# Kernel tuning notes

Hardware: AMD Instinct MI355X
Metric: run time of the kernel (lower is better)

## Reference

```python
import jax, jax.numpy as jnp
import numpy as np

N = 2_097_152  # total atoms
G = 32_768     # number of graphs (~64 atoms each)
EPS = 1e-4     # sign-detection threshold from the original code


def setup_inputs() -> dict:
    key = jax.random.key(0)
    k1, k2 = jax.random.split(key)
    pos = jax.random.normal(k1, (N, 3), dtype=jnp.float32) * 3.0
    batch = jnp.sort(jax.random.randint(k2, (N,), 0, G))
    return {"pos": pos, "batch": batch, "num_graphs": G}


def reference(pos, batch, num_graphs):
    n = pos.shape[0]
    dtype = pos.dtype

    # per-graph centroid (scatter_mean)
    counts = jax.ops.segment_sum(jnp.ones((n,), dtype), batch, num_segments=num_graphs)
    center = jax.ops.segment_sum(pos, batch, num_segments=num_graphs) / jnp.maximum(counts, 1.0)[:, None]
    pc = pos - center[batch]                      # [N,3] centered positions

    # per-atom inertia contribution: r^2 * I - p p^T, then scatter_add per graph
    r_sq = jnp.sum(pc * pc, axis=-1)              # [N]
    outer = jnp.einsum('ni,nj->nij', pc, pc)      # [N,3,3]
    I_atom = r_sq[:, None, None] * jnp.eye(3, dtype=dtype) - outer
    I_mol = jax.ops.segment_sum(I_atom, batch, num_segments=num_graphs)  # [G,3,3]

    L, Q = jnp.linalg.eigh(I_mol)                 # Q: [G,3,3], columns = principal axes

    # projections of centered positions onto the (pre-flip) eigenbasis.
    # NOTE: in the torch loop, p_proj is computed once before any sign flips, and
    # flipping column 0 does not affect p_proj[:,1], so axes 0 and 1 are independent.
    proj = jnp.einsum('ni,nij->nj', pc, Q[batch])  # [N,3]

    idx = jnp.arange(n)

    def axis_sign(a):
        # parallel "first atom (in original order) with |proj| > EPS" per graph
        qual = jnp.abs(proj[:, a]) > EPS
        key_idx = jnp.where(qual, idx, n)
        first = jax.ops.segment_min(key_idx, batch, num_segments=num_graphs)  # [G]
        found = first < n
        val = proj[jnp.minimum(first, n - 1), a]
        return jnp.where(found & (val < 0), -1.0, 1.0).astype(dtype)

    s0 = axis_sign(0)
    s1 = axis_sign(1)
    q0 = Q[:, :, 0] * s0[:, None]
    q1 = Q[:, :, 1] * s1[:, None]
    q2 = jnp.cross(q0, q1)  # enforce right-handed frame
    return jnp.stack([q0, q1, q2], axis=-1)       # [G,3,3]
```

## Files before the change

### kernel.cpp

```cpp
#include <hip/hip_runtime.h>
#include <math.h>

#define CANON_EPS 1e-4f

__global__ __launch_bounds__(256) void moments_kernel(
    const float* __restrict__ pos, const int* __restrict__ batch,
    int* __restrict__ wsi, float* __restrict__ wsf, int n, int G) {
  int tid = (int)(blockIdx.x * (unsigned)blockDim.x + threadIdx.x);
  int gid = tid >> 3;
  int sub = tid & 7;
  int lane = (int)(threadIdx.x & 63u);
  if (gid >= G) return;

  int target = gid + (sub & 1);
  int lo = 0, hi = n;
  while (lo < hi) {
    int mid = (lo + hi) >> 1;
    bool less = batch[mid] < target;
    lo = less ? mid + 1 : lo;
    hi = less ? hi : mid;
  }
  int base = lane & ~7;
  int s = __shfl(lo, base);
  int e = __shfl(lo, base + 1);
  if (sub == 0) wsi[gid] = s;
  if (sub == 1 && gid == G - 1) wsi[G] = lo;

  int cnt = e - s;

  float sx = 0.f, sy = 0.f, sz = 0.f;
  float sxx = 0.f, syy = 0.f, szz = 0.f, sxy = 0.f, sxz = 0.f, syz = 0.f;
  for (int i = s + sub; i < e; i += 8) {
    float x = pos[3 * i + 0];
    float y = pos[3 * i + 1];
    float z = pos[3 * i + 2];
    sx += x; sy += y; sz += z;
    sxx = fmaf(x, x, sxx); syy = fmaf(y, y, syy); szz = fmaf(z, z, szz);
    sxy = fmaf(x, y, sxy); sxz = fmaf(x, z, sxz); syz = fmaf(y, z, syz);
  }
#define RED8(v)                                                              \
  v += __shfl_xor(v, 1); v += __shfl_xor(v, 2); v += __shfl_xor(v, 4);
  RED8(sx) RED8(sy) RED8(sz)
  RED8(sxx) RED8(syy) RED8(szz)
  RED8(sxy) RED8(sxz) RED8(syz)
#undef RED8

  float fn = (float)(cnt > 0 ? cnt : 1);
  float inv = 1.0f / fn;
  float mx = sx * inv, my = sy * inv, mz = sz * inv;
  float Sxx = fmaf(-fn * mx, mx, sxx);
  float Syy = fmaf(-fn * my, my, syy);
  float Szz = fmaf(-fn * mz, mz, szz);
  float Sxy = fmaf(-fn * mx, my, sxy);
  float Sxz = fmaf(-fn * mx, mz, sxz);
  float Syz = fmaf(-fn * my, mz, syz);

  float v = mx;
  v = (sub == 1) ? my : v;
  v = (sub == 2) ? mz : v;
  v = (sub == 3) ? (Syy + Szz) : v;
  v = (sub == 4) ? (Sxx + Szz) : v;
  v = (sub == 5) ? (Sxx + Syy) : v;
  v = (sub == 6) ? (-Sxy) : v;
  v = (sub == 7) ? (-Sxz) : v;
  wsf[sub * G + gid] = v;
  if (sub == 0) wsf[8 * G + gid] = -Syz;
}

__device__ __forceinline__ void jacobi3_f32(float a00, float a11, float a22,
                                            float a01, float a02, float a12,
                                            float Q[3][3]) {
  float A00 = a00, A11 = a11, A22 = a22;
  float A01 = a01, A02 = a02, A12 = a12;
  float Q00 = 1.f, Q01 = 0.f, Q02 = 0.f;
  float Q10 = 0.f, Q11 = 1.f, Q12 = 0.f;
  float Q20 = 0.f, Q21 = 0.f, Q22 = 1.f;

#define ROT(App, Aqq, Apq, Akp, Akq, Qrp0, Qrq0, Qrp1, Qrq1, Qrp2, Qrq2)     \
  {                                                                          \
    float apq = Apq;                                                         \
    float theta = (Aqq - App) / (2.0f * apq);                                \
    float t = copysignf(1.0f, theta) /                                       \
              (fabsf(theta) + sqrtf(1.0f + theta * theta));                  \
    t = (apq == 0.0f) ? 0.0f : t;                    \
    float c = 1.0f / sqrtf(1.0f + t * t);                                    \
    float s = t * c;                                                         \
    App = App - t * apq;                                                     \
    Aqq = Aqq + t * apq;                                                     \
    Apq = 0.0f;                                                              \
    float akp = Akp, akq = Akq;                                              \
    Akp = c * akp - s * akq;                                                 \
    Akq = s * akp + c * akq;                                                 \
    float r0p = Qrp0, r0q = Qrq0;                                            \
    Qrp0 = c * r0p - s * r0q;                                                \
    Qrq0 = s * r0p + c * r0q;                                                \
    float r1p = Qrp1, r1q = Qrq1;                                            \
    Qrp1 = c * r1p - s * r1q;                                                \
    Qrq1 = s * r1p + c * r1q;                                                \
    float r2p = Qrp2, r2q = Qrq2;                                            \
    Qrp2 = c * r2p - s * r2q;                                                \
    Qrq2 = s * r2p + c * r2q;                                                \
  }

#pragma unroll
  for (int sweep = 0; sweep < 5; ++sweep) {
    ROT(A00, A11, A01, A02, A12, Q00, Q01, Q10, Q11, Q20, Q21);
    ROT(A00, A22, A02, A01, A12, Q00, Q02, Q10, Q12, Q20, Q22);
    ROT(A11, A22, A12, A01, A02, Q01, Q02, Q11, Q12, Q21, Q22);
  }
#undef ROT

  float w0 = A00, w1 = A11, w2 = A22;
#define CSWAP(wa, wb, qa0, qb0, qa1, qb1, qa2, qb2)                          \
  {                                                                          \
    bool sw = (wb) < (wa);                                                   \
    float tw = wa; wa = sw ? wb : wa; wb = sw ? tw : wb;                     \
    float t0 = qa0; qa0 = sw ? qb0 : qa0; qb0 = sw ? t0 : qb0;               \
    float t1 = qa1; qa1 = sw ? qb1 : qa1; qb1 = sw ? t1 : qb1;               \
    float t2 = qa2; qa2 = sw ? qb2 : qa2; qb2 = sw ? t2 : qb2;               \
  }
  CSWAP(w0, w1, Q00, Q01, Q10, Q11, Q20, Q21);
  CSWAP(w1, w2, Q01, Q02, Q11, Q12, Q21, Q22);
  CSWAP(w0, w1, Q00, Q01, Q10, Q11, Q20, Q21);
#undef CSWAP

  Q[0][0] = Q00; Q[0][1] = Q01; Q[0][2] = Q02;
  Q[1][0] = Q10; Q[1][1] = Q11; Q[1][2] = Q12;
  Q[2][0] = Q20; Q[2][1] = Q21; Q[2][2] = Q22;
}

__global__ __launch_bounds__(256) void eigen_kernel(
    const float* __restrict__ pos, const int* __restrict__ wsi,
    const float* __restrict__ wsf, float* __restrict__ out, int G) {
  int g = (int)(blockIdx.x * (unsigned)blockDim.x + threadIdx.x);
  if (g >= G) return;

  int s = wsi[g];
  int e = wsi[g + 1];

  float cx  = wsf[0 * G + g];
  float cy  = wsf[1 * G + g];
  float cz  = wsf[2 * G + g];
  float ixx = wsf[3 * G + g];
  float iyy = wsf[4 * G + g];
  float izz = wsf[5 * G + g];
  float ixy = wsf[6 * G + g];
  float ixz = wsf[7 * G + g];
  float iyz = wsf[8 * G + g];

  float Q[3][3];
  jacobi3_f32(ixx, iyy, izz, ixy, ixz, iyz, Q);

  float q00 = Q[0][0], q10 = Q[1][0], q20 = Q[2][0];
  float q01 = Q[0][1], q11 = Q[1][1], q21 = Q[2][1];

  bool found0 = false, found1 = false;
  float v0 = 0.f, v1 = 0.f;
  for (int i = s; i < e; ++i) {
    float x = pos[3 * i + 0] - cx;
    float y = pos[3 * i + 1] - cy;
    float z = pos[3 * i + 2] - cz;
    float p0 = x * q00 + y * q10 + z * q20;
    float p1 = x * q01 + y * q11 + z * q21;
    if (!found0 && fabsf(p0) > CANON_EPS) { v0 = p0; found0 = true; }
    if (!found1 && fabsf(p1) > CANON_EPS) { v1 = p1; found1 = true; }
    if (found0 && found1) break;
  }
  float s0 = (found0 && v0 < 0.f) ? -1.f : 1.f;
  float s1 = (found1 && v1 < 0.f) ? -1.f : 1.f;

  float q0x = q00 * s0, q0y = q10 * s0, q0z = q20 * s0;
  float q1x = q01 * s1, q1y = q11 * s1, q1z = q21 * s1;
  float q2x = q0y * q1z - q0z * q1y;
  float q2y = q0z * q1x - q0x * q1z;
  float q2z = q0x * q1y - q0y * q1x;
  float* o = out + (size_t)g * 9;
  o[0] = q0x; o[1] = q1x; o[2] = q2x;
  o[3] = q0y; o[4] = q1y; o[5] = q2y;
  o[6] = q0z; o[7] = q1z; o[8] = q2z;
}

extern "C" void kernel_launch(void* const* d_in, const int* in_sizes, int n_in,
                              void* d_out, int out_size, void* d_ws, size_t ws_size,
                              hipStream_t stream) {
  const float* pos = (const float*)d_in[0];
  const int* batch = (const int*)d_in[1];
  float* out = (float*)d_out;

  int n = in_sizes[0] / 3;
  int G = out_size / 9;

  int* wsi = (int*)d_ws;
  float* wsf = (float*)((char*)d_ws + (((size_t)(G + 1) * 4 + 255) & ~255ull));

  int blocksA = (G * 8 + 255) / 256;
  moments_kernel<<<blocksA, 256, 0, stream>>>(pos, batch, wsi, wsf, n, G);

  eigen_kernel<<<(G + 255) / 256, 256, 0, stream>>>(pos, wsi, wsf, out, G);
}
```

Baseline: 23.46 us.

## Replace per-graph binary search moments with atom-parallel segmented atomic accumulation

Moments are now computed by scanning atoms in fixed chunks of 16 per thread with vectorized loads. Each thread keeps running sums per segment and flushes them to per-graph accumulators with atomics, and it writes segment boundaries where the graph id changes. This removes the per-graph binary searches and the strided, poorly coalesced loads. The centroid and inertia finalization moves into the eigen kernel, which now launches with 64-thread blocks. In exchange it adds a zeroing kernel launch, atomic contention on graphs that span chunk boundaries, and float summation order that varies between runs.

After: 70.15 us. 2.99x slower.

```diff
diff --git a/kernel.cpp b/kernel.cpp
--- a/kernel.cpp
+++ b/kernel.cpp
@@ -2,69 +2,90 @@
 #include <math.h>
 
 #define CANON_EPS 1e-4f
+#define KPT 16
+
+__global__ __launch_bounds__(256) void zero_ws_kernel(float* __restrict__ wsf,
+                                                      int total) {
+  int i = (int)(blockIdx.x * (unsigned)blockDim.x + threadIdx.x);
+  if (i < total) wsf[i] = 0.0f;
+}
 
 __global__ __launch_bounds__(256) void moments_kernel(
     const float* __restrict__ pos, const int* __restrict__ batch,
     int* __restrict__ wsi, float* __restrict__ wsf, int n, int G) {
-  int tid = (int)(blockIdx.x * (unsigned)blockDim.x + threadIdx.x);
-  int gid = tid >> 3;
-  int sub = tid & 7;
-  int lane = (int)(threadIdx.x & 63u);
-  if (gid >= G) return;
-
-  int target = gid + (sub & 1);
-  int lo = 0, hi = n;
-  while (lo < hi) {
-    int mid = (lo + hi) >> 1;
-    bool less = batch[mid] < target;
-    lo = less ? mid + 1 : lo;
-    hi = less ? hi : mid;
-  }
-  int base = lane & ~7;
-  int s = __shfl(lo, base);
-  int e = __shfl(lo, base + 1);
-  if (sub == 0) wsi[gid] = s;
-  if (sub == 1 && gid == G - 1) wsi[G] = lo;
-
-  int cnt = e - s;
+  int t = (int)(blockIdx.x * (unsigned)blockDim.x + threadIdx.x);
+  int i0 = t * KPT;
+  if (i0 >= n) return;
+
+  int pb = (i0 > 0) ? batch[i0 - 1] : -1;
 
   float sx = 0.f, sy = 0.f, sz = 0.f;
   float sxx = 0.f, syy = 0.f, szz = 0.f, sxy = 0.f, sxz = 0.f, syz = 0.f;
-  for (int i = s + sub; i < e; i += 8) {
-    float x = pos[3 * i + 0];
-    float y = pos[3 * i + 1];
-    float z = pos[3 * i + 2];
-    sx += x; sy += y; sz += z;
-    sxx = fmaf(x, x, sxx); syy = fmaf(y, y, syy); szz = fmaf(z, z, szz);
-    sxy = fmaf(x, y, sxy); sxz = fmaf(x, z, sxz); syz = fmaf(y, z, syz);
-  }
-#define RED8(v)                                                              \
-  v += __shfl_xor(v, 1); v += __shfl_xor(v, 2); v += __shfl_xor(v, 4);
-  RED8(sx) RED8(sy) RED8(sz)
-  RED8(sxx) RED8(syy) RED8(szz)
-  RED8(sxy) RED8(sxz) RED8(syz)
-#undef RED8
-
-  float fn = (float)(cnt > 0 ? cnt : 1);
-  float inv = 1.0f / fn;
-  float mx = sx * inv, my = sy * inv, mz = sz * inv;
-  float Sxx = fmaf(-fn * mx, mx, sxx);
-  float Syy = fmaf(-fn * my, my, syy);
-  float Szz = fmaf(-fn * mz, mz, szz);
-  float Sxy = fmaf(-fn * mx, my, sxy);
-  float Sxz = fmaf(-fn * mx, mz, sxz);
-  float Syz = fmaf(-fn * my, mz, syz);
-
-  float v = mx;
-  v = (sub == 1) ? my : v;
-  v = (sub == 2) ? mz : v;
-  v = (sub == 3) ? (Syy + Szz) : v;
-  v = (sub == 4) ? (Sxx + Szz) : v;
-  v = (sub == 5) ? (Sxx + Syy) : v;
-  v = (sub == 6) ? (-Sxy) : v;
-  v = (sub == 7) ? (-Sxz) : v;
-  wsf[sub * G + gid] = v;
-  if (sub == 0) wsf[8 * G + gid] = -Syz;
+  int cur = pb;
+
+#define FLUSH()                                                              \
+  if (cur >= 0) {                                                            \
+    atomicAdd(&wsf[0 * G + cur], sx);                                        \
+    atomicAdd(&wsf[1 * G + cur], sy);                                        \
+    atomicAdd(&wsf[2 * G + cur], sz);                                        \
+    atomicAdd(&wsf[3 * G + cur], sxx);                                       \
+    atomicAdd(&wsf[4 * G + cur], syy);                                       \
+    atomicAdd(&wsf[5 * G + cur], szz);                                       \
+    atomicAdd(&wsf[6 * G + cur], sxy);                                       \
+    atomicAdd(&wsf[7 * G + cur], sxz);                                       \
+    atomicAdd(&wsf[8 * G + cur], syz);                                       \
+  }
+
+  if (i0 + KPT <= n) {
+    int B[KPT];
+#pragma unroll
+    for (int q = 0; q < KPT / 4; ++q) {
+      int4 b4 = *reinterpret_cast<const int4*>(batch + i0 + 4 * q);
+      B[4 * q + 0] = b4.x; B[4 * q + 1] = b4.y;
+      B[4 * q + 2] = b4.z; B[4 * q + 3] = b4.w;
+    }
+    float P[3 * KPT];
+#pragma unroll
+    for (int q = 0; q < 3 * KPT / 4; ++q) {
+      float4 p4 = *reinterpret_cast<const float4*>(pos + (size_t)3 * i0 + 4 * q);
+      P[4 * q + 0] = p4.x; P[4 * q + 1] = p4.y;
+      P[4 * q + 2] = p4.z; P[4 * q + 3] = p4.w;
+    }
+#pragma unroll
+    for (int k = 0; k < KPT; ++k) {
+      int bk = B[k];
+      if (bk != cur) {
+        for (int g = cur + 1; g <= bk; ++g) wsi[g] = i0 + k;
+        FLUSH();
+        sx = sy = sz = sxx = syy = szz = sxy = sxz = syz = 0.f;
+        cur = bk;
+      }
+      float x = P[3 * k + 0], y = P[3 * k + 1], z = P[3 * k + 2];
+      sx += x; sy += y; sz += z;
+      sxx = fmaf(x, x, sxx); syy = fmaf(y, y, syy); szz = fmaf(z, z, szz);
+      sxy = fmaf(x, y, sxy); sxz = fmaf(x, z, sxz); syz = fmaf(y, z, syz);
+    }
+  } else {
+    for (int i = i0; i < n; ++i) {
+      int bk = batch[i];
+      if (bk != cur) {
+        for (int g = cur + 1; g <= bk; ++g) wsi[g] = i;
+        FLUSH();
+        sx = sy = sz = sxx = syy = szz = sxy = sxz = syz = 0.f;
+        cur = bk;
+      }
+      float x = pos[3 * i + 0], y = pos[3 * i + 1], z = pos[3 * i + 2];
+      sx += x; sy += y; sz += z;
+      sxx = fmaf(x, x, sxx); syy = fmaf(y, y, syy); szz = fmaf(z, z, szz);
+      sxy = fmaf(x, y, sxy); sxz = fmaf(x, z, sxz); syz = fmaf(y, z, syz);
+    }
+  }
+  FLUSH();
+#undef FLUSH
+
+  if (i0 + KPT >= n) {
+    for (int g = cur + 1; g <= G; ++g) wsi[g] = n;
+  }
 }
 
 __device__ __forceinline__ void jacobi3_f32(float a00, float a11, float a22,
@@ -129,7 +150,7 @@
   Q[2][0] = Q20; Q[2][1] = Q21; Q[2][2] = Q22;
 }
 
-__global__ __launch_bounds__(256) void eigen_kernel(
+__global__ __launch_bounds__(64) void eigen_kernel(
     const float* __restrict__ pos, const int* __restrict__ wsi,
     const float* __restrict__ wsf, float* __restrict__ out, int G) {
   int g = (int)(blockIdx.x * (unsigned)blockDim.x + threadIdx.x);
@@ -137,16 +158,34 @@
 
   int s = wsi[g];
   int e = wsi[g + 1];
-
-  float cx  = wsf[0 * G + g];
-  float cy  = wsf[1 * G + g];
-  float cz  = wsf[2 * G + g];
-  float ixx = wsf[3 * G + g];
-  float iyy = wsf[4 * G + g];
-  float izz = wsf[5 * G + g];
-  float ixy = wsf[6 * G + g];
-  float ixz = wsf[7 * G + g];
-  float iyz = wsf[8 * G + g];
+  int cnt = e - s;
+
+  float sx  = wsf[0 * G + g];
+  float sy  = wsf[1 * G + g];
+  float sz  = wsf[2 * G + g];
+  float sxx = wsf[3 * G + g];
+  float syy = wsf[4 * G + g];
+  float szz = wsf[5 * G + g];
+  float sxy = wsf[6 * G + g];
+  float sxz = wsf[7 * G + g];
+  float syz = wsf[8 * G + g];
+
+  float fn = (float)(cnt > 0 ? cnt : 1);
+  float inv = 1.0f / fn;
+  float mx = sx * inv, my = sy * inv, mz = sz * inv;
+  float Sxx = fmaf(-fn * mx, mx, sxx);
+  float Syy = fmaf(-fn * my, my, syy);
+  float Szz = fmaf(-fn * mz, mz, szz);
+  float Sxy = fmaf(-fn * mx, my, sxy);
+  float Sxz = fmaf(-fn * mx, mz, sxz);
+  float Syz = fmaf(-fn * my, mz, syz);
+
+  float ixx = Syy + Szz;
+  float iyy = Sxx + Szz;
+  float izz = Sxx + Syy;
+  float ixy = -Sxy;
+  float ixz = -Sxz;
+  float iyz = -Syz;
 
   float Q[3][3];
   jacobi3_f32(ixx, iyy, izz, ixy, ixz, iyz, Q);
@@ -157,9 +196,9 @@
   bool found0 = false, found1 = false;
   float v0 = 0.f, v1 = 0.f;
   for (int i = s; i < e; ++i) {
-    float x = pos[3 * i + 0] - cx;
-    float y = pos[3 * i + 1] - cy;
-    float z = pos[3 * i + 2] - cz;
+    float x = pos[3 * i + 0] - mx;
+    float y = pos[3 * i + 1] - my;
+    float z = pos[3 * i + 2] - mz;
     float p0 = x * q00 + y * q10 + z * q20;
     float p1 = x * q01 + y * q11 + z * q21;
     if (!found0 && fabsf(p0) > CANON_EPS) { v0 = p0; found0 = true; }
@@ -193,8 +232,12 @@
   int* wsi = (int*)d_ws;
   float* wsf = (float*)((char*)d_ws + (((size_t)(G + 1) * 4 + 255) & ~255ull));
 
-  int blocksA = (G * 8 + 255) / 256;
-  moments_kernel<<<blocksA, 256, 0, stream>>>(pos, batch, wsi, wsf, n, G);
-
-  eigen_kernel<<<(G + 255) / 256, 256, 0, stream>>>(pos, wsi, wsf, out, G);
-}
+  int totalf = 9 * G;
+  zero_ws_kernel<<<(totalf + 255) / 256, 256, 0, stream>>>(wsf, totalf);
+
+  int threadsA = (n + KPT - 1) / KPT;
+  moments_kernel<<<(threadsA + 255) / 256, 256, 0, stream>>>(pos, batch, wsi,
+                                                             wsf, n, G);
+
+  eigen_kernel<<<(G + 63) / 64, 64, 0, stream>>>(pos, wsi, wsf, out, G);
+}
```

## Precompute segment starts in a scan kernel and widen per-graph moment reduction

Applied to the files above, without the earlier changes.

Replaces the per-graph binary search over batch with a separate kernel that writes segment start offsets by comparing adjacent batch entries. The moments kernel now uses 16 lanes per graph with a predicated, unrolled first pass, and the eigen kernel's sign search loads atoms four at a time. This removes dependent search latency but adds a full pass over batch and an extra kernel launch.

Result: faster. 22.73 us (-3.1%).

```diff
diff --git a/kernel.cpp b/kernel.cpp
--- a/kernel.cpp
+++ b/kernel.cpp
@@ -3,34 +3,47 @@
 
 #define CANON_EPS 1e-4f
 
+__global__ __launch_bounds__(256) void build_starts_kernel(
+    const int* __restrict__ batch, int* __restrict__ wsi, int n, int G) {
+  int i = (int)(blockIdx.x * (unsigned)blockDim.x + threadIdx.x);
+  if (i >= n) return;
+  int b = batch[i];
+  int bp = (i == 0) ? -1 : batch[i - 1];
+  for (int g = bp + 1; g <= b; ++g) wsi[g] = i;
+  if (i == n - 1) {
+    for (int g = b + 1; g <= G; ++g) wsi[G > g ? g : G] = n;
+  }
+}
+
 __global__ __launch_bounds__(256) void moments_kernel(
-    const float* __restrict__ pos, const int* __restrict__ batch,
-    int* __restrict__ wsi, float* __restrict__ wsf, int n, int G) {
+    const float* __restrict__ pos, const int* __restrict__ wsi,
+    float* __restrict__ wsf, int G) {
   int tid = (int)(blockIdx.x * (unsigned)blockDim.x + threadIdx.x);
-  int gid = tid >> 3;
-  int sub = tid & 7;
-  int lane = (int)(threadIdx.x & 63u);
+  int gid = tid >> 4;
+  int sub = tid & 15;
   if (gid >= G) return;
 
-  int target = gid + (sub & 1);
-  int lo = 0, hi = n;
-  while (lo < hi) {
-    int mid = (lo + hi) >> 1;
-    bool less = batch[mid] < target;
-    lo = less ? mid + 1 : lo;
-    hi = less ? hi : mid;
-  }
-  int base = lane & ~7;
-  int s = __shfl(lo, base);
-  int e = __shfl(lo, base + 1);
-  if (sub == 0) wsi[gid] = s;
-  if (sub == 1 && gid == G - 1) wsi[G] = lo;
-
+  int s = wsi[gid];
+  int e = wsi[gid + 1];
   int cnt = e - s;
 
   float sx = 0.f, sy = 0.f, sz = 0.f;
   float sxx = 0.f, syy = 0.f, szz = 0.f, sxy = 0.f, sxz = 0.f, syz = 0.f;
-  for (int i = s + sub; i < e; i += 8) {
+
+#pragma unroll
+  for (int k = 0; k < 5; ++k) {
+    int i = s + sub + 16 * k;
+    bool in = i < e;
+    int ii = in ? i : s;
+    float m = in ? 1.0f : 0.0f;
+    float x = pos[3 * ii + 0] * m;
+    float y = pos[3 * ii + 1] * m;
+    float z = pos[3 * ii + 2] * m;
+    sx += x; sy += y; sz += z;
+    sxx = fmaf(x, x, sxx); syy = fmaf(y, y, syy); szz = fmaf(z, z, szz);
+    sxy = fmaf(x, y, sxy); sxz = fmaf(x, z, sxz); syz = fmaf(y, z, syz);
+  }
+  for (int i = s + 80 + sub; i < e; i += 16) {
     float x = pos[3 * i + 0];
     float y = pos[3 * i + 1];
     float z = pos[3 * i + 2];
@@ -38,12 +51,14 @@
     sxx = fmaf(x, x, sxx); syy = fmaf(y, y, syy); szz = fmaf(z, z, szz);
     sxy = fmaf(x, y, sxy); sxz = fmaf(x, z, sxz); syz = fmaf(y, z, syz);
   }
-#define RED8(v)                                                              \
-  v += __shfl_xor(v, 1); v += __shfl_xor(v, 2); v += __shfl_xor(v, 4);
-  RED8(sx) RED8(sy) RED8(sz)
-  RED8(sxx) RED8(syy) RED8(szz)
-  RED8(sxy) RED8(sxz) RED8(syz)
-#undef RED8
+
+#define RED16(v)                                                             \
+  v += __shfl_xor(v, 1); v += __shfl_xor(v, 2);                              \
+  v += __shfl_xor(v, 4); v += __shfl_xor(v, 8);
+  RED16(sx) RED16(sy) RED16(sz)
+  RED16(sxx) RED16(syy) RED16(szz)
+  RED16(sxy) RED16(sxz) RED16(syz)
+#undef RED16
 
   float fn = (float)(cnt > 0 ? cnt : 1);
   float inv = 1.0f / fn;
@@ -63,7 +78,7 @@
   v = (sub == 5) ? (Sxx + Syy) : v;
   v = (sub == 6) ? (-Sxy) : v;
   v = (sub == 7) ? (-Sxz) : v;
-  wsf[sub * G + gid] = v;
+  if (sub < 8) wsf[sub * G + gid] = v;
   if (sub == 0) wsf[8 * G + gid] = -Syz;
 }
 
@@ -156,15 +171,29 @@
 
   bool found0 = false, found1 = false;
   float v0 = 0.f, v1 = 0.f;
-  for (int i = s; i < e; ++i) {
-    float x = pos[3 * i + 0] - cx;
-    float y = pos[3 * i + 1] - cy;
-    float z = pos[3 * i + 2] - cz;
-    float p0 = x * q00 + y * q10 + z * q20;
-    float p1 = x * q01 + y * q11 + z * q21;
-    if (!found0 && fabsf(p0) > CANON_EPS) { v0 = p0; found0 = true; }
-    if (!found1 && fabsf(p1) > CANON_EPS) { v1 = p1; found1 = true; }
-    if (found0 && found1) break;
+  for (int base = s; base < e && !(found0 && found1); base += 4) {
+    float px[4], py[4], pz[4];
+    bool iv[4];
+#pragma unroll
+    for (int j = 0; j < 4; ++j) {
+      int i = base + j;
+      bool in = i < e;
+      iv[j] = in;
+      int ii = in ? i : s;
+      px[j] = pos[3 * ii + 0];
+      py[j] = pos[3 * ii + 1];
+      pz[j] = pos[3 * ii + 2];
+    }
+#pragma unroll
+    for (int j = 0; j < 4; ++j) {
+      if (iv[j]) {
+        float x = px[j] - cx, y = py[j] - cy, z = pz[j] - cz;
+        float p0 = x * q00 + y * q10 + z * q20;
+        float p1 = x * q01 + y * q11 + z * q21;
+        if (!found0 && fabsf(p0) > CANON_EPS) { v0 = p0; found0 = true; }
+        if (!found1 && fabsf(p1) > CANON_EPS) { v1 = p1; found1 = true; }
+      }
+    }
   }
   float s0 = (found0 && v0 < 0.f) ? -1.f : 1.f;
   float s1 = (found1 && v1 < 0.f) ? -1.f : 1.f;
@@ -193,8 +222,9 @@
   int* wsi = (int*)d_ws;
   float* wsf = (float*)((char*)d_ws + (((size_t)(G + 1) * 4 + 255) & ~255ull));
 
-  int blocksA = (G * 8 + 255) / 256;
-  moments_kernel<<<blocksA, 256, 0, stream>>>(pos, batch, wsi, wsf, n, G);
+  build_starts_kernel<<<(n + 255) / 256, 256, 0, stream>>>(batch, wsi, n, G);
+
+  moments_kernel<<<(G * 16 + 255) / 256, 256, 0, stream>>>(pos, wsi, wsf, G);
 
   eigen_kernel<<<(G + 255) / 256, 256, 0, stream>>>(pos, wsi, wsf, out, G);
 }
```
